# Kernel tuning notes

Hardware: AMD Instinct MI355X
Metric: run time of the kernel (lower is better)

The kernel has to match this reference:

```python
import jax, jax.numpy as jnp
import numpy as np

D_MODEL = 1024
NUM_HEADS = 16
D_HEAD = D_MODEL // NUM_HEADS
NEG_BIG = 10000000000.0  # matches the torch module's -1e10 mask constant


def setup_inputs() -> dict:
    key = jax.random.key(0)
    ks = jax.random.split(key, 9)
    d = D_MODEL
    scale = 1.0 / np.sqrt(d)
    inp = {
        "x": jax.random.normal(ks[0], (2, 2048, d), dtype=jnp.float32),
        "W_q": jax.random.normal(ks[1], (d, d), dtype=jnp.float32) * scale,
        "b_q": jnp.zeros((d,), dtype=jnp.float32),
        "W_k": jax.random.normal(ks[2], (d, d), dtype=jnp.float32) * scale,
        "b_k": jnp.zeros((d,), dtype=jnp.float32),
        "W_v": jax.random.normal(ks[3], (d, d), dtype=jnp.float32) * scale,
        "b_v": jnp.zeros((d,), dtype=jnp.float32),
        "W_o": jax.random.normal(ks[4], (d, d), dtype=jnp.float32) * scale,
        "b_o": jnp.zeros((d,), dtype=jnp.float32),
    }
    return inp


def reference(x, W_q, b_q, W_k, b_k, W_v, b_v, W_o, b_o):
    B, S, d = x.shape
    H, Dh = NUM_HEADS, D_HEAD

    Q = x @ W_q + b_q  # [B,S,d]
    K = x @ W_k + b_k
    V = x @ W_v + b_v

    # split heads: [B,S,d] -> [B,H,S,Dh]
    Qh = Q.reshape(B, S, H, Dh).transpose(0, 2, 1, 3)
    Kh = K.reshape(B, S, H, Dh).transpose(0, 2, 1, 3)
    Vh = V.reshape(B, S, H, Dh).transpose(0, 2, 1, 3)

    scores = jnp.einsum("bhid,bhjd->bhij", Qh, Kh) / jnp.sqrt(
        jnp.asarray(Dh, dtype=x.dtype)
    )

    # causal mask: tril(scores) - 1e10 * (1 - tril_mask)
    causal = jnp.tril(jnp.ones((S, S), dtype=x.dtype))
    scores = scores * causal - NEG_BIG * (1.0 - causal)

    attn = jax.nn.softmax(scores, axis=-1)  # dropout p=0.0 -> identity

    vals = jnp.einsum("bhij,bhjd->bhid", attn, Vh)  # [B,H,S,Dh]
    vals = vals.transpose(0, 2, 1, 3).reshape(B, S, d)

    return vals @ W_o + b_o
```

## Files before the change

kernel.cpp:

```cpp
#include <hip/hip_runtime.h>

typedef unsigned short u16;
typedef __attribute__((ext_vector_type(8))) short short8;
typedef __attribute__((ext_vector_type(4))) short shortx4;
typedef __attribute__((ext_vector_type(4))) float floatx4;

#define S_ 2048
#define D_ 1024
#define DQKV_ 3072
#define H_ 16
#define DH_ 64

#define EXP2F(x) __builtin_amdgcn_exp2f(x)

template <bool B> struct BoolC { static constexpr bool value = B; };

__device__ __forceinline__ float bf2f(u16 x) {
    union { unsigned int u; float f; } v; v.u = ((unsigned int)x) << 16; return v.f;
}
__device__ __forceinline__ u16 f2bf(float f) {
    unsigned int u = __float_as_uint(f);
    return (u16)((u + 0x7fffu + ((u >> 16) & 1u)) >> 16);
}
__device__ __forceinline__ unsigned int cvtpk_bf16(float lo, float hi) {
    unsigned int r;
    asm("v_cvt_pk_bf16_f32 %0, %1, %2" : "=v"(r) : "v"(lo), "v"(hi));
    return r;
}

__device__ __forceinline__ void async16(const void* g, void* l) {
    __builtin_amdgcn_global_load_lds(
        (const __attribute__((address_space(1))) unsigned int*)g,
        (__attribute__((address_space(3))) unsigned int*)l, 16, 0, 0);
}

__global__ __launch_bounds__(256) void convert_x(const float* __restrict__ x, u16* __restrict__ xb) {
    const size_t i = ((size_t)blockIdx.x * 256 + threadIdx.x) * 4;
    float4 v = *(const float4*)&x[i];
    shortx4 h;
    h[0] = (short)f2bf(v.x); h[1] = (short)f2bf(v.y);
    h[2] = (short)f2bf(v.z); h[3] = (short)f2bf(v.w);
    *(shortx4*)&xb[i] = h;
}

__global__ __launch_bounds__(256) void transpose_w4(const float* __restrict__ Wq, const float* __restrict__ Wk,
                                                    const float* __restrict__ Wv, const float* __restrict__ Wo,
                                                    u16* __restrict__ Wqkvt, u16* __restrict__ Wot) {
    __shared__ u16 tile[32][33];
    const int z = blockIdx.z;
    const float* W = (z == 0) ? Wq : (z == 1) ? Wk : (z == 2) ? Wv : Wo;
    u16* dst = (z == 3) ? Wot : (Wqkvt + (size_t)z * D_ * D_);
    const int tx = threadIdx.x, ty = threadIdx.y;
    const int n0 = blockIdx.x * 32, k0 = blockIdx.y * 32;
#pragma unroll
    for (int r = 0; r < 4; ++r) {
        int k = ty + r * 8;
        tile[k][tx] = f2bf(W[(size_t)(k0 + k) * D_ + n0 + tx]);
    }
    __syncthreads();
#pragma unroll
    for (int r = 0; r < 4; ++r) {
        int n = ty + r * 8;
        dst[(size_t)(n0 + n) * D_ + k0 + tx] = tile[tx][n];
    }
}

__global__ __launch_bounds__(256) void transpose_headV(const u16* __restrict__ QKV, u16* __restrict__ Vt) {
    __shared__ u16 tile[64 * 65];
    const int t = threadIdx.x;
    const int bh = blockIdx.y, b = bh >> 4, h = bh & 15;
    const int s0 = blockIdx.x << 6;
#pragma unroll
    for (int i = 0; i < 16; ++i) {
        int idx = t + (i << 8);
        int s = idx >> 6, d = idx & 63;
        tile[s * 65 + d] = QKV[(size_t)(b * S_ + s0 + s) * DQKV_ + 2048 + h * DH_ + d];
    }
    __syncthreads();
#pragma unroll
    for (int i = 0; i < 16; ++i) {
        int idx = t + (i << 8);
        int d = idx >> 6, p = idx & 63;
        int sk = ((p >> 5) << 5) | (((p >> 2) & 1) << 4) | (((p >> 3) & 3) << 2) | (p & 3);
        Vt[((size_t)bh * DH_ + d) * S_ + s0 + p] = tile[sk * 65 + d];
    }
}

template <int BM, int BN, bool OUTF32>
__global__ __launch_bounds__(256) void gemm_bt(const u16* __restrict__ A, const u16* __restrict__ Bt,
                                               const float* __restrict__ b0, const float* __restrict__ b1,
                                               const float* __restrict__ b2, void* __restrict__ Cp,
                                               int M, int N, int Kd) {
    constexpr int FI = BM / 32, FJ = BN / 32;
    __shared__ __align__(16) u16 smem[2][(BM + BN) * 32];
    const int t = threadIdx.x;

    const int nwg = gridDim.x * gridDim.y;
    int fid = blockIdx.y * gridDim.x + blockIdx.x;
    if ((nwg & 7) == 0) fid = (fid & 7) * (nwg >> 3) + (fid >> 3);
    const int bx = fid % gridDim.x, by = fid / gridDim.x;
    const int m0 = by * BM, n0 = bx * BN;

    const int w = t >> 6, lane = t & 63;
    const int lr = lane & 15, lg = lane >> 4;
    const int wm = (w >> 1) * (BM / 2), wn = (w & 1) * (BN / 2);
    const int srow = lane >> 2, scol = (lane & 3) << 3;
    floatx4 acc[FI][FJ] = {};

    auto stage = [&](int buf, int k0) {
        u16* As = &smem[buf][0];
        u16* Bs = &smem[buf][BM * 32];
#pragma unroll
        for (int c = 0; c < BM / 64; ++c) {
            int rbase = (w * (BM / 64) + c) * 16;
            async16(&A[(size_t)(m0 + rbase + srow) * Kd + k0 + scol], &As[rbase * 32]);
        }
#pragma unroll
        for (int c = 0; c < BN / 64; ++c) {
            int rbase = (w * (BN / 64) + c) * 16;
            async16(&Bt[(size_t)(n0 + rbase + srow) * Kd + k0 + scol], &Bs[rbase * 32]);
        }
    };

    stage(0, 0);
    const int nk = Kd / 32;
    for (int kk = 0; kk < nk; ++kk) {
        const int cur = kk & 1;
        __syncthreads();
        if (kk + 1 < nk) stage(cur ^ 1, (kk + 1) * 32);
        const u16* As = &smem[cur][0];
        const u16* Bs = &smem[cur][BM * 32];

        short8 af[FI], bfr[FJ];
#pragma unroll
        for (int i = 0; i < FI; ++i) af[i]  = *(const short8*)&As[(wm + i * 16 + lr) * 32 + lg * 8];
#pragma unroll
        for (int j = 0; j < FJ; ++j) bfr[j] = *(const short8*)&Bs[(wn + j * 16 + lr) * 32 + lg * 8];
#pragma unroll
        for (int i = 0; i < FI; ++i)
#pragma unroll
            for (int j = 0; j < FJ; ++j)
                acc[i][j] = __builtin_amdgcn_mfma_f32_16x16x32_bf16(af[i], bfr[j], acc[i][j], 0, 0, 0);
    }

    if (!OUTF32) {
        __syncthreads();
        u16* Cs = &smem[0][0];
#pragma unroll
        for (int j = 0; j < FJ; ++j) {
            int c = wn + j * 16 + lr;
            int col = n0 + c;
            const float* bp = (col < 1024) ? b0 : (col < 2048) ? b1 : b2;
            float bv = bp[col & 1023];
#pragma unroll
            for (int i = 0; i < FI; ++i)
#pragma unroll
                for (int ii = 0; ii < 4; ++ii) {
                    int r = wm + i * 16 + lg * 4 + ii;
                    Cs[r * BN + (c ^ ((r & 15) << 3))] = f2bf(acc[i][j][ii] + bv);
                }
        }
        __syncthreads();
        constexpr int CPR = BN / 8;
        constexpr int ITER = BM * CPR / 256;
#pragma unroll
        for (int it = 0; it < ITER; ++it) {
            int g = it * 256 + t;
            int r = g / CPR, cc = g % CPR;
            short8 vv = *(const short8*)&Cs[r * BN + ((cc * 8) ^ ((r & 15) << 3))];
            *(short8*)((u16*)Cp + (size_t)(m0 + r) * N + n0 + cc * 8) = vv;
        }
    } else {
#pragma unroll
        for (int j = 0; j < FJ; ++j) {
            int col = n0 + wn + j * 16 + lr;
            const float* bp = (col < 1024) ? b0 : (col < 2048) ? b1 : b2;
            float bv = bp[col & 1023];
#pragma unroll
            for (int i = 0; i < FI; ++i) {
                int rb = m0 + wm + i * 16 + lg * 4;
#pragma unroll
                for (int ii = 0; ii < 4; ++ii)
                    ((float*)Cp)[(size_t)(rb + ii) * N + col] = acc[i][j][ii] + bv;
            }
        }
    }
}

__global__ __launch_bounds__(256, 4) void attn_mfma(const u16* __restrict__ QKV, const u16* __restrict__ Vt,
                                                    u16* __restrict__ O) {
    __shared__ __align__(16) u16 KsA[2][64 * 64];
    __shared__ __align__(16) u16 VsA[2][64 * 64];
    const int t = threadIdx.x, w = t >> 6, lane = t & 63;
    const int lr = lane & 15, lg = lane >> 4;
    const int wq = w & 1, wk = w >> 1;
    const int bh = blockIdx.x, b = bh >> 4, h = bh & 15;
    const int ya = blockIdx.y & 7, yb = blockIdx.y >> 3;
    const int a4 = (ya + 4) & 7;
    const int cq = (yb == 0) ? ya : (yb == 1) ? (7 - ya) : (yb == 2) ? a4 : (7 - a4);
    const int qt = (yb << 3) + cq;
    const int q0 = qt << 6;
    const float cs = 0.18033688f;

    const u16* Kb  = QKV + (size_t)b * S_ * DQKV_ + 1024 + h * DH_;
    const u16* Vtb = Vt + (size_t)bh * DH_ * S_;

    const int rb8 = lane >> 3;
    const int cc = ((lane & 7) ^ rb8) << 3;
    const int swz = lr & 7;

    short8 qf[2][2];
#pragma unroll
    for (int qs = 0; qs < 2; ++qs)
#pragma unroll
        for (int ks = 0; ks < 2; ++ks)
            qf[qs][ks] = *(const short8*)&QKV[(size_t)(b * S_ + q0 + wq * 32 + qs * 16 + lr) * DQKV_ +
                                              h * DH_ + ks * 32 + lg * 8];

    floatx4 of[2][4] = {};
    float lsum[2] = {0.f, 0.f};

    auto stage = [&](int buf, int kbase) {
        u16* Kd = &KsA[buf][w * 512];
        u16* Vd = &VsA[buf][w * 512];
        async16(&Kb[(size_t)(kbase + w * 8 + rb8) * DQKV_ + cc], Kd);
        async16(&Kb[(size_t)(kbase + 32 + w * 8 + rb8) * DQKV_ + cc], Kd + 2048);
        async16(&Vtb[(size_t)(w * 8 + rb8) * S_ + kbase + cc], Vd);
        async16(&Vtb[(size_t)(32 + w * 8 + rb8) * S_ + kbase + cc], Vd + 2048);
    };

    stage(0, 0);

    auto body = [&](int kb, auto diagc) {
        constexpr bool DIAG = decltype(diagc)::value;
        const int cur = kb & 1;
        __syncthreads();
        if (kb < qt) stage(cur ^ 1, (kb + 1) << 6);
        const u16* Kc = KsA[cur];
        const u16* Vc = VsA[cur];

        floatx4 sf[2][2] = {};
        __builtin_amdgcn_s_setprio(1);
#pragma unroll
        for (int ks = 0; ks < 2; ++ks)
#pragma unroll
            for (int tt = 0; tt < 2; ++tt) {
                short8 kf = *(const short8*)&Kc[(wk * 32 + tt * 16 + lr) * 64 + ((((ks << 2) + lg) ^ swz) << 3)];
                sf[0][tt] = __builtin_amdgcn_mfma_f32_16x16x32_bf16(kf, qf[0][ks], sf[0][tt], 0, 0, 0);
                sf[1][tt] = __builtin_amdgcn_mfma_f32_16x16x32_bf16(kf, qf[1][ks], sf[1][tt], 0, 0, 0);
            }
        __builtin_amdgcn_s_setprio(0);

        float ev[2][2][4];
#pragma unroll
        for (int qs = 0; qs < 2; ++qs)
#pragma unroll
            for (int tt = 0; tt < 2; ++tt) {
                float s0;
#pragma unroll
                for (int ii = 0; ii < 4; ++ii) {
                    float e = EXP2F(sf[qs][tt][ii] * cs);
                    if (DIAG && (wk * 32 + tt * 16 + lg * 4 + ii > wq * 32 + qs * 16 + lr)) e = 0.f;
                    ev[qs][tt][ii] = e;
                    s0 = (ii == 0) ? e : s0 + e;
                }
                lsum[qs] += s0;
            }

        short8 vfr[4];
#pragma unroll
        for (int ttd = 0; ttd < 4; ++ttd)
            vfr[ttd] = *(const short8*)&Vc[(ttd * 16 + lr) * 64 + ((((wk << 2) + lg) ^ swz) << 3)];
        __builtin_amdgcn_s_setprio(1);
#pragma unroll
        for (int qs = 0; qs < 2; ++qs) {
            union { short8 s; unsigned int u[4]; } pk;
            pk.u[0] = cvtpk_bf16(ev[qs][0][0], ev[qs][0][1]);
            pk.u[1] = cvtpk_bf16(ev[qs][0][2], ev[qs][0][3]);
            pk.u[2] = cvtpk_bf16(ev[qs][1][0], ev[qs][1][1]);
            pk.u[3] = cvtpk_bf16(ev[qs][1][2], ev[qs][1][3]);
#pragma unroll
            for (int ttd = 0; ttd < 4; ++ttd)
                of[qs][ttd] = __builtin_amdgcn_mfma_f32_16x16x32_bf16(pk.s, vfr[ttd], of[qs][ttd], 0, 0, 0);
        }
        __builtin_amdgcn_s_setprio(0);
    };

    for (int kb = 0; kb < qt; ++kb) body(kb, BoolC<false>{});
    body(qt, BoolC<true>{});

    __syncthreads();
    float* mb = (float*)&KsA[0][0];
    float* lb = (float*)&VsA[0][0];
    if (wk == 1) {
        float* mw = mb + wq * 2048;
#pragma unroll
        for (int qs = 0; qs < 2; ++qs)
#pragma unroll
            for (int ttd = 0; ttd < 4; ++ttd)
                *(floatx4*)&mw[(qs * 4 + ttd) * 256 + lane * 4] = of[qs][ttd];
        lb[wq * 128 + lane * 2 + 0] = lsum[0];
        lb[wq * 128 + lane * 2 + 1] = lsum[1];
    }
    __syncthreads();
    if (wk == 0) {
        float* mw = mb + wq * 2048;
#pragma unroll
        for (int qs = 0; qs < 2; ++qs)
#pragma unroll
            for (int ttd = 0; ttd < 4; ++ttd)
                of[qs][ttd] += *(const floatx4*)&mw[(qs * 4 + ttd) * 256 + lane * 4];
        lsum[0] += lb[wq * 128 + lane * 2 + 0];
        lsum[1] += lb[wq * 128 + lane * 2 + 1];

        float rv[2][4];
#pragma unroll
        for (int qs = 0; qs < 2; ++qs) {
            float s = lsum[qs];
            s += __shfl_xor(s, 16);
            s += __shfl_xor(s, 32);
            float rinv = 1.f / s;
#pragma unroll
            for (int ii = 0; ii < 4; ++ii)
                rv[qs][ii] = __shfl(rinv, (lane & 48) | (lg * 4 + ii));
        }
#pragma unroll
        for (int qs = 0; qs < 2; ++qs)
#pragma unroll
            for (int ttd = 0; ttd < 4; ++ttd)
#pragma unroll
                for (int ii = 0; ii < 4; ++ii)
                    O[(size_t)(b * S_ + q0 + wq * 32 + qs * 16 + lg * 4 + ii) * D_ + h * DH_ + ttd * 16 + lr] =
                        f2bf(of[qs][ttd][ii] * rv[qs][ii]);
    }
}

extern "C" void kernel_launch(void* const* d_in, const int* in_sizes, int n_in,
                              void* d_out, int out_size, void* d_ws, size_t ws_size,
                              hipStream_t stream) {
    (void)in_sizes; (void)n_in; (void)out_size; (void)ws_size;
    const float* x  = (const float*)d_in[0];
    const float* Wq = (const float*)d_in[1];
    const float* bq = (const float*)d_in[2];
    const float* Wk = (const float*)d_in[3];
    const float* bk = (const float*)d_in[4];
    const float* Wv = (const float*)d_in[5];
    const float* bv = (const float*)d_in[6];
    const float* Wo = (const float*)d_in[7];
    const float* bo = (const float*)d_in[8];

    u16* ws    = (u16*)d_ws;
    u16* WqkvT = ws;
    u16* WoT   = ws + (size_t)3 * (1 << 20);
    u16* QKV   = ws + (size_t)4 * (1 << 20);
    u16* Vtm   = ws + (size_t)16 * (1 << 20);
    u16* xbf   = ws + (size_t)20 * (1 << 20);
    u16* Am    = ws + (size_t)20 * (1 << 20);

    convert_x<<<4096, 256, 0, stream>>>(x, xbf);
    transpose_w4<<<dim3(32, 32, 4), dim3(32, 8), 0, stream>>>(Wq, Wk, Wv, Wo, WqkvT, WoT);

    gemm_bt<128, 128, false><<<dim3(DQKV_ / 128, 4096 / 128), 256, 0, stream>>>(
        xbf, WqkvT, bq, bk, bv, QKV, 4096, DQKV_, 1024);

    transpose_headV<<<dim3(32, 32), 256, 0, stream>>>(QKV, Vtm);

    attn_mfma<<<dim3(32, 32), 256, 0, stream>>>(QKV, Vtm, Am);

    gemm_bt<64, 128, true><<<dim3(1024 / 128, 4096 / 64), 256, 0, stream>>>(
        Am, WoT, bo, bo, bo, d_out, 4096, 1024, 1024);
}
```

Measured before the change: 178.5 us.

## Fuse V head-transpose into QKV GEMM epilogue and merge prep kernels

```diff
diff --git a/kernel.cpp b/kernel.cpp
--- a/kernel.cpp
+++ b/kernel.cpp
@@ -34,23 +34,26 @@
         (__attribute__((address_space(3))) unsigned int*)l, 16, 0, 0);
 }
 
-__global__ __launch_bounds__(256) void convert_x(const float* __restrict__ x, u16* __restrict__ xb) {
-    const size_t i = ((size_t)blockIdx.x * 256 + threadIdx.x) * 4;
-    float4 v = *(const float4*)&x[i];
-    shortx4 h;
-    h[0] = (short)f2bf(v.x); h[1] = (short)f2bf(v.y);
-    h[2] = (short)f2bf(v.z); h[3] = (short)f2bf(v.w);
-    *(shortx4*)&xb[i] = h;
-}
-
-__global__ __launch_bounds__(256) void transpose_w4(const float* __restrict__ Wq, const float* __restrict__ Wk,
-                                                    const float* __restrict__ Wv, const float* __restrict__ Wo,
-                                                    u16* __restrict__ Wqkvt, u16* __restrict__ Wot) {
+__global__ __launch_bounds__(256) void prep(const float* __restrict__ x,
+                                            const float* __restrict__ Wq, const float* __restrict__ Wk,
+                                            const float* __restrict__ Wv, const float* __restrict__ Wo,
+                                            u16* __restrict__ xb, u16* __restrict__ Wqkvt, u16* __restrict__ Wot) {
     __shared__ u16 tile[32][33];
     const int z = blockIdx.z;
+    const int tx = threadIdx.x, ty = threadIdx.y;
+    if (z >= 4) {
+        const int t = ty * 32 + tx;
+        const size_t bid = (size_t)(z - 4) * 1024 + blockIdx.y * 32 + blockIdx.x;
+        const size_t i = (bid * 256 + t) * 4;
+        float4 v = *(const float4*)&x[i];
+        shortx4 h;
+        h[0] = (short)f2bf(v.x); h[1] = (short)f2bf(v.y);
+        h[2] = (short)f2bf(v.z); h[3] = (short)f2bf(v.w);
+        *(shortx4*)&xb[i] = h;
+        return;
+    }
     const float* W = (z == 0) ? Wq : (z == 1) ? Wk : (z == 2) ? Wv : Wo;
     u16* dst = (z == 3) ? Wot : (Wqkvt + (size_t)z * D_ * D_);
-    const int tx = threadIdx.x, ty = threadIdx.y;
     const int n0 = blockIdx.x * 32, k0 = blockIdx.y * 32;
 #pragma unroll
     for (int r = 0; r < 4; ++r) {
@@ -62,27 +65,6 @@
     for (int r = 0; r < 4; ++r) {
         int n = ty + r * 8;
         dst[(size_t)(n0 + n) * D_ + k0 + tx] = tile[tx][n];
-    }
-}
-
-__global__ __launch_bounds__(256) void transpose_headV(const u16* __restrict__ QKV, u16* __restrict__ Vt) {
-    __shared__ u16 tile[64 * 65];
-    const int t = threadIdx.x;
-    const int bh = blockIdx.y, b = bh >> 4, h = bh & 15;
-    const int s0 = blockIdx.x << 6;
-#pragma unroll
-    for (int i = 0; i < 16; ++i) {
-        int idx = t + (i << 8);
-        int s = idx >> 6, d = idx & 63;
-        tile[s * 65 + d] = QKV[(size_t)(b * S_ + s0 + s) * DQKV_ + 2048 + h * DH_ + d];
-    }
-    __syncthreads();
-#pragma unroll
-    for (int i = 0; i < 16; ++i) {
-        int idx = t + (i << 8);
-        int d = idx >> 6, p = idx & 63;
-        int sk = ((p >> 5) << 5) | (((p >> 2) & 1) << 4) | (((p >> 3) & 3) << 2) | (p & 3);
-        Vt[((size_t)bh * DH_ + d) * S_ + s0 + p] = tile[sk * 65 + d];
     }
 }
 
@@ -90,7 +72,7 @@
 __global__ __launch_bounds__(256) void gemm_bt(const u16* __restrict__ A, const u16* __restrict__ Bt,
                                                const float* __restrict__ b0, const float* __restrict__ b1,
                                                const float* __restrict__ b2, void* __restrict__ Cp,
-                                               int M, int N, int Kd) {
+                                               u16* __restrict__ Vt, int M, int N, int Kd) {
     constexpr int FI = BM / 32, FJ = BN / 32;
     __shared__ __align__(16) u16 smem[2][(BM + BN) * 32];
     const int t = threadIdx.x;
@@ -146,29 +128,60 @@
     if (!OUTF32) {
         __syncthreads();
         u16* Cs = &smem[0][0];
-#pragma unroll
-        for (int j = 0; j < FJ; ++j) {
-            int c = wn + j * 16 + lr;
-            int col = n0 + c;
-            const float* bp = (col < 1024) ? b0 : (col < 2048) ? b1 : b2;
-            float bv = bp[col & 1023];
-#pragma unroll
-            for (int i = 0; i < FI; ++i)
-#pragma unroll
-                for (int ii = 0; ii < 4; ++ii) {
-                    int r = wm + i * 16 + lg * 4 + ii;
-                    Cs[r * BN + (c ^ ((r & 15) << 3))] = f2bf(acc[i][j][ii] + bv);
+        if (BM == BN && n0 >= 2048) {
+            const int bb = m0 >> 11;
+            const int s_in = m0 & 2047;
+            const int h0 = (n0 - 2048) >> 6;
+#pragma unroll
+            for (int j = 0; j < FJ; ++j) {
+                int c = wn + j * 16 + lr;
+                float bv = b2[(n0 + c) & 1023];
+#pragma unroll
+                for (int i = 0; i < FI; ++i) {
+                    int r = wm + i * 16 + lg * 4;
+                    int s6 = r & 63;
+                    int P = (r & ~63) | (s6 & 32) | (((s6 >> 3) & 1) << 4) | (((s6 >> 2) & 1) << 3)
+                          | (((s6 >> 4) & 1) << 2);
+                    shortx4 pk4;
+#pragma unroll
+                    for (int ii = 0; ii < 4; ++ii) pk4[ii] = (short)f2bf(acc[i][j][ii] + bv);
+                    *(shortx4*)&Cs[c * BM + (P ^ ((c & 15) << 3))] = pk4;
                 }
-        }
-        __syncthreads();
-        constexpr int CPR = BN / 8;
-        constexpr int ITER = BM * CPR / 256;
-#pragma unroll
-        for (int it = 0; it < ITER; ++it) {
-            int g = it * 256 + t;
-            int r = g / CPR, cc = g % CPR;
-            short8 vv = *(const short8*)&Cs[r * BN + ((cc * 8) ^ ((r & 15) << 3))];
-            *(short8*)((u16*)Cp + (size_t)(m0 + r) * N + n0 + cc * 8) = vv;
+            }
+            __syncthreads();
+#pragma unroll
+            for (int it = 0; it < (BM * BN / 8) / 256; ++it) {
+                int ch = t & 15;
+                int dl = it * 16 + (t >> 4);
+                short8 vv = *(const short8*)&Cs[dl * BM + ((ch * 8) ^ ((dl & 15) << 3))];
+                int hh = h0 + (dl >> 6), d = dl & 63;
+                *(short8*)&Vt[((size_t)((bb * 16 + hh) * 64 + d)) * (size_t)S_ + s_in + ch * 8] = vv;
+            }
+        } else {
+#pragma unroll
+            for (int j = 0; j < FJ; ++j) {
+                int c = wn + j * 16 + lr;
+                int col = n0 + c;
+                const float* bp = (col < 1024) ? b0 : (col < 2048) ? b1 : b2;
+                float bv = bp[col & 1023];
+#pragma unroll
+                for (int i = 0; i < FI; ++i)
+#pragma unroll
+                    for (int ii = 0; ii < 4; ++ii) {
+                        int r = wm + i * 16 + lg * 4 + ii;
+                        Cs[r * BN + (c ^ ((r & 15) << 3))] = f2bf(acc[i][j][ii] + bv);
+                    }
+            }
+            __syncthreads();
+            constexpr int CPR = BN / 8;
+            constexpr int ITER = BM * CPR / 256;
+#pragma unroll
+            for (int it = 0; it < ITER; ++it) {
+                int g = it * 256 + t;
+                int r = g / CPR, cc = g % CPR;
+                short8 vv = *(const short8*)&Cs[r * BN + ((cc * 8) ^ ((r & 15) << 3))];
+                *(short8*)((u16*)Cp + (size_t)(m0 + r) * N + n0 + cc * 8) = vv;
+            }
         }
     } else {
 #pragma unroll
@@ -357,16 +370,13 @@
     u16* xbf   = ws + (size_t)20 * (1 << 20);
     u16* Am    = ws + (size_t)20 * (1 << 20);
 
-    convert_x<<<4096, 256, 0, stream>>>(x, xbf);
-    transpose_w4<<<dim3(32, 32, 4), dim3(32, 8), 0, stream>>>(Wq, Wk, Wv, Wo, WqkvT, WoT);
+    prep<<<dim3(32, 32, 8), dim3(32, 8), 0, stream>>>(x, Wq, Wk, Wv, Wo, xbf, WqkvT, WoT);
 
     gemm_bt<128, 128, false><<<dim3(DQKV_ / 128, 4096 / 128), 256, 0, stream>>>(
-        xbf, WqkvT, bq, bk, bv, QKV, 4096, DQKV_, 1024);
-
-    transpose_headV<<<dim3(32, 32), 256, 0, stream>>>(QKV, Vtm);
+        xbf, WqkvT, bq, bk, bv, QKV, Vtm, 4096, DQKV_, 1024);
 
     attn_mfma<<<dim3(32, 32), 256, 0, stream>>>(QKV, Vtm, Am);
 
     gemm_bt<64, 128, true><<<dim3(1024 / 128, 4096 / 64), 256, 0, stream>>>(
-        Am, WoT, bo, bo, bo, d_out, 4096, 1024, 1024);
-}
+        Am, WoT, bo, bo, bo, d_out, nullptr, 4096, 1024, 1024);
+}
```

Measured after the change: 179.1 us. About the same (+0.3%).
